# Performance work log

Measured on AMD Instinct MI355X. Metric: run time of the kernel, lower is better.

## Reference

```python
import jax, jax.numpy as jnp
import numpy as np
import math

B, D, S, H = 4, 1024, 2048, 16


def setup_inputs() -> dict:
    key = jax.random.key(0)
    ks = jax.random.split(key, 9)
    scale = 0.02
    return {
        "x": jax.random.normal(ks[0], (B, D, S), dtype=jnp.float32),
        "Wq": jax.random.normal(ks[1], (D, D), dtype=jnp.float32) * scale,
        "bq": jnp.zeros((D,), dtype=jnp.float32),
        "Wk": jax.random.normal(ks[2], (D, D), dtype=jnp.float32) * scale,
        "bk": jnp.zeros((D,), dtype=jnp.float32),
        "Wv": jax.random.normal(ks[3], (D, D), dtype=jnp.float32) * scale,
        "bv": jnp.zeros((D,), dtype=jnp.float32),
        "Wo": jax.random.normal(ks[4], (D, D), dtype=jnp.float32) * scale,
        "bo": jnp.zeros((D,), dtype=jnp.float32),
        "num_heads": H,
    }


def _positional_encoding(d_model, seq_len):
    # pe[0::2, :] = sin(pos * denom), pe[1::2, :] = cos(pos * denom)
    pos = jnp.arange(seq_len, dtype=jnp.float32)[None, :]            # [1, S]
    denom = jnp.exp(jnp.arange(0, d_model, 2, dtype=jnp.float32)
                    * (-math.log(10000.0) / d_model))[:, None]        # [D/2, 1]
    angles = pos * denom                                              # [D/2, S]
    pe = jnp.zeros((d_model, seq_len), dtype=jnp.float32)
    pe = pe.at[0::2, :].set(jnp.sin(angles))
    pe = pe.at[1::2, :].set(jnp.cos(angles))
    return pe


def reference(x, Wq, bq, Wk, bk, Wv, bv, Wo, bo, num_heads):
    b, d_model, s = x.shape
    head_dim = d_model // num_heads
    x = x + _positional_encoding(d_model, s)[None, :, :]  # broadcast over batch
    x = jnp.transpose(x, (0, 2, 1))                       # [B, S, D]
    q = x @ Wq.T + bq
    k = x @ Wk.T + bk
    v = x @ Wv.T + bv
    # [B, S, H, hd] -> [B, H, S, hd]
    q = q.reshape(b, s, num_heads, head_dim).transpose(0, 2, 1, 3)
    k = k.reshape(b, s, num_heads, head_dim).transpose(0, 2, 1, 3)
    v = v.reshape(b, s, num_heads, head_dim).transpose(0, 2, 1, 3)
    scores = jnp.einsum('bhqd,bhkd->bhqk', q, k) / jnp.sqrt(
        jnp.asarray(head_dim, dtype=jnp.float32))
    attn = jax.nn.softmax(scores, axis=-1)
    out = jnp.einsum('bhqk,bhkd->bhqd', attn, v)          # [B, H, S, hd]
    out = out.transpose(0, 2, 1, 3).reshape(b, s, d_model)
    out = out @ Wo.T + bo
    return jnp.transpose(out, (0, 2, 1))                  # [B, D, S]
```

## Files before the change

kernel.cpp:

```cpp
#include <hip/hip_runtime.h>


typedef __bf16 bf16;
typedef __attribute__((ext_vector_type(8))) __bf16 bf16x8;
typedef __attribute__((ext_vector_type(4))) __bf16 bf16x4;
typedef __attribute__((ext_vector_type(4))) float f32x4;

#define NB 4
#define ND 1024
#define NS 2048
#define NH 16
#define NM 8192

__device__ __forceinline__ void gld16(const void* g, void* l) {
  __builtin_amdgcn_global_load_lds((__attribute__((address_space(1))) void*)g,
                                   (__attribute__((address_space(3))) void*)l, 16, 0, 0);
}

__device__ __forceinline__ int swz4(int r) { return (r + (r >> 2)) & 3; }

__device__ __forceinline__ float exp2_fast(float x) {
#if __has_builtin(__builtin_amdgcn_exp2f)
  return __builtin_amdgcn_exp2f(x);
#else
  return exp2f(x);
#endif
}

__global__ __launch_bounds__(256) void prep_x_kernel(const float* __restrict__ x,
                                                     bf16* __restrict__ xT) {
  __shared__ float t[32][33];
  const int tx = threadIdx.x, ty = threadIdx.y;
  const int s0 = blockIdx.x * 32, d0 = blockIdx.y * 32, b = blockIdx.z;
#pragma unroll
  for (int i = 0; i < 4; ++i) {
    const int rr = ty + i * 8;
    const int d = d0 + rr, s = s0 + tx;
    const float freq = __expf(-(float)(d >> 1) * 0.01798894603980689f);
    const float ang = (float)s * freq;
    const float pe = (d & 1) ? cosf(ang) : sinf(ang);
    t[rr][tx] = x[((size_t)b * ND + d) * NS + s] + pe;
  }
  __syncthreads();
#pragma unroll
  for (int i = 0; i < 4; ++i) {
    const int a = ty + i * 8;
    xT[((size_t)b * NS + s0 + a) * ND + d0 + tx] = (bf16)t[tx][a];
  }
}

__global__ __launch_bounds__(256) void prep_w_kernel(const float* __restrict__ Wq,
                                                     const float* __restrict__ Wk,
                                                     const float* __restrict__ Wv,
                                                     const float* __restrict__ Wo,
                                                     bf16* __restrict__ Wqkv,
                                                     bf16* __restrict__ WoB) {
  const size_t t = (size_t)blockIdx.x * blockDim.x + threadIdx.x;
  const size_t i = t * 4;
  const float* src;
  bf16* dst;
  size_t off;
  if (i < (size_t)3 * 1024 * 1024) {
    const int sel = (int)(i >> 20);
    src = sel == 0 ? Wq : (sel == 1 ? Wk : Wv);
    off = i - ((size_t)sel << 20);
    dst = Wqkv + i;
  } else {
    src = Wo;
    off = i - ((size_t)3 << 20);
    dst = WoB + off;
  }
  const f32x4 v = *(const f32x4*)(src + off);
  bf16x4 o;
  o[0] = (bf16)v[0];
  o[1] = (bf16)v[1];
  o[2] = (bf16)v[2];
  o[3] = (bf16)v[3];
  *(bf16x4*)dst = o;
}

__device__ __forceinline__ void gemm_tile_128(const bf16* __restrict__ A,
                                              const bf16* __restrict__ Bm,
                                              int tm, int tn, bf16* ldsA, bf16* ldsB,
                                              f32x4 acc[4][4]) {
  const int tid = threadIdx.x;
  const int lane = tid & 63, wave = tid >> 6;
  const int wm = wave >> 1, wn = wave & 1;
  const int rl = lane & 15, quad = lane >> 4;
  const int sw = swz4(rl);
  int r0[2], c0[2], ld0[2];
#pragma unroll
  for (int j = 0; j < 2; ++j) {
    const int chunk = wave * 2 + j;
    const int o = chunk * 1024 + lane * 16;
    const int r = o >> 6;
    r0[j] = r;
    c0[j] = (((o >> 4) & 3) ^ swz4(r)) * 8;
    ld0[j] = chunk * 1024;
  }
  for (int kt = 0; kt < 1024; kt += 32) {
#pragma unroll
    for (int j = 0; j < 2; ++j) {
      gld16(A + (size_t)(tm + r0[j]) * 1024 + kt + c0[j], (char*)ldsA + ld0[j]);
      gld16(Bm + (size_t)(tn + r0[j]) * 1024 + kt + c0[j], (char*)ldsB + ld0[j]);
    }
    __syncthreads();
    bf16x8 af[4], bfr[4];
#pragma unroll
    for (int i = 0; i < 4; ++i) {
      const int ra = wm * 64 + i * 16 + rl;
      af[i] = *(const bf16x8*)((const char*)ldsA + ra * 64 + ((quad ^ sw) * 16));
      const int rb = wn * 64 + i * 16 + rl;
      bfr[i] = *(const bf16x8*)((const char*)ldsB + rb * 64 + ((quad ^ sw) * 16));
    }
#pragma unroll
    for (int i = 0; i < 4; ++i)
#pragma unroll
      for (int j = 0; j < 4; ++j)
        acc[i][j] = __builtin_amdgcn_mfma_f32_16x16x32_bf16(af[i], bfr[j], acc[i][j], 0, 0, 0);
    __syncthreads();
  }
}

__global__ __launch_bounds__(256, 2) void gemm_qkv_kernel(
    const bf16* __restrict__ xT, const bf16* __restrict__ Wqkv,
    const float* __restrict__ bq, const float* __restrict__ bk,
    const float* __restrict__ bv, bf16* __restrict__ Q, bf16* __restrict__ Kb,
    bf16* __restrict__ VT) {
  __shared__ bf16 ldsA[128 * 32], ldsB[128 * 32];
  const int tm = blockIdx.x * 128, tn = blockIdx.y * 128;
  f32x4 acc[4][4];
  const f32x4 z = {0.f, 0.f, 0.f, 0.f};
#pragma unroll
  for (int i = 0; i < 4; ++i)
#pragma unroll
    for (int j = 0; j < 4; ++j) acc[i][j] = z;
  gemm_tile_128(xT, Wqkv, tm, tn, ldsA, ldsB, acc);
  const int lane = threadIdx.x & 63, wave = threadIdx.x >> 6;
  const int wm = wave >> 1, wn = wave & 1;
  const int rl = lane & 15, quad = lane >> 4;
  const float QSCALE = 0.18033688011112042f;
#pragma unroll
  for (int j = 0; j < 4; ++j) {
    const int n = tn + wn * 64 + j * 16 + rl;
    const int which = n >> 10;
    const int nl = n & 1023;
    const int h = nl >> 6, d = nl & 63;
    const float bias = (which == 0 ? bq : which == 1 ? bk : bv)[nl];
#pragma unroll
    for (int i = 0; i < 4; ++i) {
      const int m0 = tm + wm * 64 + i * 16 + quad * 4;
      const int b = m0 >> 11, s0 = m0 & 2047;
      const size_t bh = (size_t)(b * 16 + h);
      if (which == 2) {
        bf16x4 pk;
#pragma unroll
        for (int r = 0; r < 4; ++r) pk[r] = (bf16)(acc[i][j][r] + bias);
        *(bf16x4*)(VT + ((size_t)bh * 64 + d) * 2048 + s0) = pk;
      } else {
#pragma unroll
        for (int r = 0; r < 4; ++r) {
          const float v = acc[i][j][r] + bias;
          const int s = s0 + r;
          if (which == 0)
            Q[(bh * 2048 + s) * 64 + d] = (bf16)(v * QSCALE);
          else
            Kb[(bh * 2048 + s) * 64 + d] = (bf16)v;
        }
      }
    }
  }
}

__global__ __launch_bounds__(256, 2) void attn_kernel(const bf16* __restrict__ Q,
                                                      const bf16* __restrict__ Kb,
                                                      const bf16* __restrict__ VT,
                                                      bf16* __restrict__ AO) {
  __shared__ __align__(16) char smem[65536];
  char* ldsK = smem;
  char* ldsV = smem + 16384;
  char* ldsP = smem + 32768;
  const int tid = threadIdx.x;
  const int lane = tid & 63, wave = tid >> 6;
  const int rl = lane & 15, quad = lane >> 4;
  const int bh = blockIdx.y;
  const int q0 = blockIdx.x * 256;
  const bf16* Qb = Q + ((size_t)bh * 2048 + q0) * 64;
  const bf16* Kbb = Kb + (size_t)bh * 2048 * 64;
  const bf16* Vb = VT + (size_t)bh * 64 * 2048;
  const int o0 = wave * 1024 + lane * 16, o1 = o0 + 4096;
  const int ra = o0 >> 7, rb = o1 >> 7;
  const int ca = (((o0 >> 4) & 7) ^ (ra & 7)) * 16;
  const int cb = (((o1 >> 4) & 7) ^ (rb & 7)) * 16;
  gld16((const char*)Kbb + (size_t)ra * 128 + ca, ldsK + wave * 1024);
  gld16((const char*)Kbb + (size_t)rb * 128 + cb, ldsK + wave * 1024 + 4096);
  gld16((const char*)Vb + (size_t)ra * 4096 + ca, ldsV + wave * 1024);
  gld16((const char*)Vb + (size_t)rb * 4096 + cb, ldsV + wave * 1024 + 4096);
  bf16x8 qf[4][2];
#pragma unroll
  for (int i = 0; i < 4; ++i)
#pragma unroll
    for (int ks = 0; ks < 2; ++ks)
      qf[i][ks] = *(const bf16x8*)(Qb + (wave * 64 + i * 16 + rl) * 64 + ks * 32 + quad * 8);
  f32x4 o_acc[4][4], lacc[4];
  const f32x4 z = {0.f, 0.f, 0.f, 0.f};
#pragma unroll
  for (int i = 0; i < 4; ++i) {
    lacc[i] = z;
#pragma unroll
    for (int j = 0; j < 4; ++j) o_acc[i][j] = z;
  }
  const bf16 oneb = (bf16)1.0f;
  const bf16x8 onesb = {oneb, oneb, oneb, oneb, oneb, oneb, oneb, oneb};
  char* Pw = ldsP + wave * 8192;
  int buf = 0;
  for (int kt = 0; kt < 2048; kt += 64, buf ^= 1) {
    __syncthreads();
    if (kt + 64 < 2048) {
      const int nb = (buf ^ 1) * 8192;
      gld16((const char*)Kbb + (size_t)(kt + 64 + ra) * 128 + ca, ldsK + nb + wave * 1024);
      gld16((const char*)Kbb + (size_t)(kt + 64 + rb) * 128 + cb,
            ldsK + nb + wave * 1024 + 4096);
      gld16((const char*)Vb + (size_t)ra * 4096 + (size_t)(kt + 64) * 2 + ca,
            ldsV + nb + wave * 1024);
      gld16((const char*)Vb + (size_t)rb * 4096 + (size_t)(kt + 64) * 2 + cb,
            ldsV + nb + wave * 1024 + 4096);
    }
    f32x4 sacc[4][4];
#pragma unroll
    for (int jk = 0; jk < 4; ++jk)
#pragma unroll
      for (int i = 0; i < 4; ++i) sacc[jk][i] = z;
#pragma unroll
    for (int ks = 0; ks < 2; ++ks) {
#pragma unroll
      for (int jk = 0; jk < 4; ++jk) {
        const bf16x8 kf = *(const bf16x8*)(ldsK + buf * 8192 + (jk * 16 + rl) * 128 +
                                           (((ks * 4 + quad) ^ (rl & 7)) * 16));
#pragma unroll
        for (int i = 0; i < 4; ++i)
          sacc[jk][i] =
              __builtin_amdgcn_mfma_f32_16x16x32_bf16(kf, qf[i][ks], sacc[jk][i], 0, 0, 0);
      }
    }
#pragma unroll
    for (int i = 0; i < 4; ++i)
#pragma unroll
      for (int jk = 0; jk < 4; ++jk) {
        bf16x4 pk;
#pragma unroll
        for (int r = 0; r < 4; ++r) pk[r] = (bf16)exp2_fast(sacc[jk][i][r]);
        *(bf16x4*)(Pw + (i * 16 + rl) * 128 +
                   (((jk * 2 + (quad >> 1)) ^ (rl & 7)) * 16) + (quad & 1) * 8) = pk;
      }
    asm volatile("s_waitcnt lgkmcnt(0)" ::: "memory");
#pragma unroll
    for (int ks = 0; ks < 2; ++ks) {
      bf16x8 pf[4];
#pragma unroll
      for (int i = 0; i < 4; ++i)
        pf[i] = *(const bf16x8*)(Pw + (i * 16 + rl) * 128 +
                                 (((ks * 4 + quad) ^ (rl & 7)) * 16));
#pragma unroll
      for (int i = 0; i < 4; ++i)
        lacc[i] = __builtin_amdgcn_mfma_f32_16x16x32_bf16(pf[i], onesb, lacc[i], 0, 0, 0);
#pragma unroll
      for (int j = 0; j < 4; ++j) {
        const bf16x8 vf = *(const bf16x8*)(ldsV + buf * 8192 + (j * 16 + rl) * 128 +
                                           (((ks * 4 + quad) ^ (rl & 7)) * 16));
#pragma unroll
        for (int i = 0; i < 4; ++i)
          o_acc[i][j] =
              __builtin_amdgcn_mfma_f32_16x16x32_bf16(pf[i], vf, o_acc[i][j], 0, 0, 0);
      }
    }
  }
  const int b = bh >> 4, h = bh & 15;
#pragma unroll
  for (int i = 0; i < 4; ++i) {
    f32x4 linv;
#pragma unroll
    for (int r = 0; r < 4; ++r) linv[r] = __builtin_amdgcn_rcpf(lacc[i][r]);
#pragma unroll
    for (int j = 0; j < 4; ++j)
#pragma unroll
      for (int r = 0; r < 4; ++r) {
        const int s = q0 + wave * 64 + i * 16 + quad * 4 + r;
        const int d = h * 64 + j * 16 + rl;
        AO[((size_t)b * 2048 + s) * 1024 + d] = (bf16)(o_acc[i][j][r] * linv[r]);
      }
  }
}

__global__ __launch_bounds__(256, 2) void gemm_out_kernel(const bf16* __restrict__ AO,
                                                          const bf16* __restrict__ WoB,
                                                          const float* __restrict__ bo,
                                                          float* __restrict__ out) {
  __shared__ bf16 ldsA[128 * 32], ldsB[128 * 32];
  const int tm = blockIdx.x * 128, tn = blockIdx.y * 128;
  f32x4 acc[4][4];
  const f32x4 z = {0.f, 0.f, 0.f, 0.f};
#pragma unroll
  for (int i = 0; i < 4; ++i)
#pragma unroll
    for (int j = 0; j < 4; ++j) acc[i][j] = z;
  gemm_tile_128(AO, WoB, tm, tn, ldsA, ldsB, acc);
  const int lane = threadIdx.x & 63, wave = threadIdx.x >> 6;
  const int wm = wave >> 1, wn = wave & 1;
  const int rl = lane & 15, quad = lane >> 4;
#pragma unroll
  for (int j = 0; j < 4; ++j) {
    const int n = tn + wn * 64 + j * 16 + rl;
    const float bias = bo[n];
#pragma unroll
    for (int i = 0; i < 4; ++i) {
      const int m0 = tm + wm * 64 + i * 16 + quad * 4;
      const int b = m0 >> 11, s = m0 & 2047;
      f32x4 v = acc[i][j];
      v[0] += bias;
      v[1] += bias;
      v[2] += bias;
      v[3] += bias;
      *(f32x4*)(out + ((size_t)(b * 1024 + n)) * 2048 + s) = v;
    }
  }
}

extern "C" void kernel_launch(void* const* d_in, const int* in_sizes, int n_in,
                              void* d_out, int out_size, void* d_ws, size_t ws_size,
                              hipStream_t stream) {
  const float* x = (const float*)d_in[0];
  const float* Wq = (const float*)d_in[1];
  const float* bq = (const float*)d_in[2];
  const float* Wk = (const float*)d_in[3];
  const float* bk = (const float*)d_in[4];
  const float* Wv = (const float*)d_in[5];
  const float* bv = (const float*)d_in[6];
  const float* Wo = (const float*)d_in[7];
  const float* bo = (const float*)d_in[8];
  float* out = (float*)d_out;

  char* p = (char*)d_ws;
  bf16* xT = (bf16*)p;
  p += (size_t)NM * ND * 2;
  bf16* Wqkv = (bf16*)p;
  p += (size_t)3 * ND * ND * 2;
  bf16* WoB = (bf16*)p;
  p += (size_t)ND * ND * 2;
  bf16* Qb = (bf16*)p;
  p += (size_t)NM * ND * 2;
  bf16* Kbf = (bf16*)p;
  p += (size_t)NM * ND * 2;
  bf16* VTb = (bf16*)p;
  p += (size_t)NM * ND * 2;
  bf16* AO = xT;

  prep_x_kernel<<<dim3(NS / 32, ND / 32, NB), dim3(32, 8), 0, stream>>>(x, xT);
  prep_w_kernel<<<dim3(4096), dim3(256), 0, stream>>>(Wq, Wk, Wv, Wo, Wqkv, WoB);
  gemm_qkv_kernel<<<dim3(NM / 128, 3072 / 128), dim3(256), 0, stream>>>(
      xT, Wqkv, bq, bk, bv, Qb, Kbf, VTb);
  attn_kernel<<<dim3(NS / 256, NB * NH), dim3(256), 0, stream>>>(Qb, Kbf, VTb, AO);
  gemm_out_kernel<<<dim3(NM / 128, ND / 128), dim3(256), 0, stream>>>(AO, WoB, bo, out);
}
```

Measured before the change: 286.1 us.

## Keep softmax probabilities in registers and use transposed PV MFMA in attention

The attention kernel no longer round-trips the exp'd scores through LDS. It computes S^T tiles so the MFMA output layout feeds directly as the B operand of a 16x16x16 bf16 MFMA computing O^T = V^T P^T, and it accumulates row sums with VALU adds plus cross-lane shuffles instead of a ones-vector MFMA. LDS use drops from 64KB to 32KB, which may raise occupancy, and the grid axes are swapped so blocks of the same query tile sit near each other. The output stores are vectorised as 4-element bf16 writes. The trade-off is the smaller-K MFMA (16 instead of 32), more PV instructions, and higher register pressure from holding P.

```diff
diff --git a/kernel.cpp b/kernel.cpp
--- a/kernel.cpp
+++ b/kernel.cpp
@@ -5,6 +5,7 @@
 typedef __attribute__((ext_vector_type(8))) __bf16 bf16x8;
 typedef __attribute__((ext_vector_type(4))) __bf16 bf16x4;
 typedef __attribute__((ext_vector_type(4))) float f32x4;
+typedef __attribute__((ext_vector_type(4))) short s16x4;
 
 #define NB 4
 #define ND 1024
@@ -176,15 +177,14 @@
                                                       const bf16* __restrict__ Kb,
                                                       const bf16* __restrict__ VT,
                                                       bf16* __restrict__ AO) {
-  __shared__ __align__(16) char smem[65536];
+  __shared__ __align__(16) char smem[32768];
   char* ldsK = smem;
   char* ldsV = smem + 16384;
-  char* ldsP = smem + 32768;
   const int tid = threadIdx.x;
   const int lane = tid & 63, wave = tid >> 6;
   const int rl = lane & 15, quad = lane >> 4;
-  const int bh = blockIdx.y;
-  const int q0 = blockIdx.x * 256;
+  const int bh = blockIdx.x;
+  const int q0 = blockIdx.y * 256;
   const bf16* Qb = Q + ((size_t)bh * 2048 + q0) * 64;
   const bf16* Kbb = Kb + (size_t)bh * 2048 * 64;
   const bf16* Vb = VT + (size_t)bh * 64 * 2048;
@@ -202,17 +202,15 @@
 #pragma unroll
     for (int ks = 0; ks < 2; ++ks)
       qf[i][ks] = *(const bf16x8*)(Qb + (wave * 64 + i * 16 + rl) * 64 + ks * 32 + quad * 8);
-  f32x4 o_acc[4][4], lacc[4];
+  f32x4 o_acc[4][4];
+  f32x4 l4[4];
   const f32x4 z = {0.f, 0.f, 0.f, 0.f};
 #pragma unroll
   for (int i = 0; i < 4; ++i) {
-    lacc[i] = z;
+    l4[i] = z;
 #pragma unroll
     for (int j = 0; j < 4; ++j) o_acc[i][j] = z;
   }
-  const bf16 oneb = (bf16)1.0f;
-  const bf16x8 onesb = {oneb, oneb, oneb, oneb, oneb, oneb, oneb, oneb};
-  char* Pw = ldsP + wave * 8192;
   int buf = 0;
   for (int kt = 0; kt < 2048; kt += 64, buf ^= 1) {
     __syncthreads();
@@ -226,69 +224,62 @@
       gld16((const char*)Vb + (size_t)rb * 4096 + (size_t)(kt + 64) * 2 + cb,
             ldsV + nb + wave * 1024 + 4096);
     }
-    f32x4 sacc[4][4];
-#pragma unroll
-    for (int jk = 0; jk < 4; ++jk)
-#pragma unroll
-      for (int i = 0; i < 4; ++i) sacc[jk][i] = z;
-#pragma unroll
-    for (int ks = 0; ks < 2; ++ks) {
-#pragma unroll
-      for (int jk = 0; jk < 4; ++jk) {
+    s16x4 pb[4][4];
+#pragma unroll
+    for (int jk = 0; jk < 4; ++jk) {
+      f32x4 sacc[4];
+#pragma unroll
+      for (int i = 0; i < 4; ++i) sacc[i] = z;
+#pragma unroll
+      for (int ks = 0; ks < 2; ++ks) {
         const bf16x8 kf = *(const bf16x8*)(ldsK + buf * 8192 + (jk * 16 + rl) * 128 +
                                            (((ks * 4 + quad) ^ (rl & 7)) * 16));
 #pragma unroll
         for (int i = 0; i < 4; ++i)
-          sacc[jk][i] =
-              __builtin_amdgcn_mfma_f32_16x16x32_bf16(kf, qf[i][ks], sacc[jk][i], 0, 0, 0);
+          sacc[i] =
+              __builtin_amdgcn_mfma_f32_16x16x32_bf16(kf, qf[i][ks], sacc[i], 0, 0, 0);
       }
-    }
-#pragma unroll
-    for (int i = 0; i < 4; ++i)
-#pragma unroll
-      for (int jk = 0; jk < 4; ++jk) {
+#pragma unroll
+      for (int i = 0; i < 4; ++i) {
+        f32x4 e;
+#pragma unroll
+        for (int r = 0; r < 4; ++r) e[r] = exp2_fast(sacc[i][r]);
+        l4[i] += e;
         bf16x4 pk;
 #pragma unroll
-        for (int r = 0; r < 4; ++r) pk[r] = (bf16)exp2_fast(sacc[jk][i][r]);
-        *(bf16x4*)(Pw + (i * 16 + rl) * 128 +
-                   (((jk * 2 + (quad >> 1)) ^ (rl & 7)) * 16) + (quad & 1) * 8) = pk;
+        for (int r = 0; r < 4; ++r) pk[r] = (bf16)e[r];
+        pb[jk][i] = __builtin_bit_cast(s16x4, pk);
       }
-    asm volatile("s_waitcnt lgkmcnt(0)" ::: "memory");
-#pragma unroll
-    for (int ks = 0; ks < 2; ++ks) {
-      bf16x8 pf[4];
-#pragma unroll
-      for (int i = 0; i < 4; ++i)
-        pf[i] = *(const bf16x8*)(Pw + (i * 16 + rl) * 128 +
-                                 (((ks * 4 + quad) ^ (rl & 7)) * 16));
-#pragma unroll
-      for (int i = 0; i < 4; ++i)
-        lacc[i] = __builtin_amdgcn_mfma_f32_16x16x32_bf16(pf[i], onesb, lacc[i], 0, 0, 0);
-#pragma unroll
-      for (int j = 0; j < 4; ++j) {
-        const bf16x8 vf = *(const bf16x8*)(ldsV + buf * 8192 + (j * 16 + rl) * 128 +
-                                           (((ks * 4 + quad) ^ (rl & 7)) * 16));
-#pragma unroll
-        for (int i = 0; i < 4; ++i)
-          o_acc[i][j] =
-              __builtin_amdgcn_mfma_f32_16x16x32_bf16(pf[i], vf, o_acc[i][j], 0, 0, 0);
+    }
+#pragma unroll
+    for (int ki = 0; ki < 4; ++ki) {
+#pragma unroll
+      for (int dt = 0; dt < 4; ++dt) {
+        const s16x4 vf = *(const s16x4*)(ldsV + buf * 8192 + (dt * 16 + rl) * 128 +
+                                         (((ki * 2 + (quad >> 1)) ^ (rl & 7)) * 16) +
+                                         (quad & 1) * 8);
+#pragma unroll
+        for (int qt = 0; qt < 4; ++qt)
+          o_acc[dt][qt] = __builtin_amdgcn_mfma_f32_16x16x16bf16_1k(vf, pb[ki][qt],
+                                                                    o_acc[dt][qt], 0, 0, 0);
       }
     }
   }
   const int b = bh >> 4, h = bh & 15;
 #pragma unroll
-  for (int i = 0; i < 4; ++i) {
-    f32x4 linv;
-#pragma unroll
-    for (int r = 0; r < 4; ++r) linv[r] = __builtin_amdgcn_rcpf(lacc[i][r]);
-#pragma unroll
-    for (int j = 0; j < 4; ++j)
-#pragma unroll
-      for (int r = 0; r < 4; ++r) {
-        const int s = q0 + wave * 64 + i * 16 + quad * 4 + r;
-        const int d = h * 64 + j * 16 + rl;
-        AO[((size_t)b * 2048 + s) * 1024 + d] = (bf16)(o_acc[i][j][r] * linv[r]);
-      }
+  for (int qt = 0; qt < 4; ++qt) {
+    float s = l4[qt][0] + l4[qt][1] + l4[qt][2] + l4[qt][3];
+    s += __shfl_xor(s, 16);
+    s += __shfl_xor(s, 32);
+    const float linv = __builtin_amdgcn_rcpf(s);
+    const size_t row = ((size_t)b * 2048 + q0 + wave * 64 + qt * 16 + rl) * 1024;
+#pragma unroll
+    for (int dt = 0; dt < 4; ++dt) {
+      bf16x4 ov;
+#pragma unroll
+      for (int r = 0; r < 4; ++r) ov[r] = (bf16)(o_acc[dt][qt][r] * linv);
+      *(bf16x4*)(AO + row + h * 64 + dt * 16 + quad * 4) = ov;
+    }
   }
 }
 
@@ -359,6 +350,6 @@
   prep_w_kernel<<<dim3(4096), dim3(256), 0, stream>>>(Wq, Wk, Wv, Wo, Wqkv, WoB);
   gemm_qkv_kernel<<<dim3(NM / 128, 3072 / 128), dim3(256), 0, stream>>>(
       xT, Wqkv, bq, bk, bv, Qb, Kbf, VTb);
-  attn_kernel<<<dim3(NS / 256, NB * NH), dim3(256), 0, stream>>>(Qb, Kbf, VTb, AO);
+  attn_kernel<<<dim3(NB * NH, NS / 256), dim3(256), 0, stream>>>(Qb, Kbf, VTb, AO);
   gemm_out_kernel<<<dim3(NM / 128, ND / 128), dim3(256), 0, stream>>>(AO, WoB, bo, out);
 }
```

New measurement: 289.4 us. About the same (+1.2%).

## Deepen GEMM K-tile to 64, interleave QK exp, and swap attention grid order

Applied to the files above, without the earlier changes.

The shared GEMM tile now loads a K-slab of 64 instead of 32 per iteration, using an 8-way XOR swizzle on 128-byte rows. This halves the number of barrier pairs per tile at the cost of twice the LDS per block. In the attention kernel, each 16x16 score tile is computed and exponentiated immediately instead of holding all 16 score accumulators first, which lowers register pressure. The attention grid is also transposed so that consecutive blocks take different heads for the same query range, which changes how K/V reads are spread across the cache.

```diff
diff --git a/kernel.cpp b/kernel.cpp
--- a/kernel.cpp
+++ b/kernel.cpp
@@ -16,8 +16,6 @@
   __builtin_amdgcn_global_load_lds((__attribute__((address_space(1))) void*)g,
                                    (__attribute__((address_space(3))) void*)l, 16, 0, 0);
 }
-
-__device__ __forceinline__ int swz4(int r) { return (r + (r >> 2)) & 3; }
 
 __device__ __forceinline__ float exp2_fast(float x) {
 #if __has_builtin(__builtin_amdgcn_exp2f)
@@ -87,37 +85,40 @@
   const int lane = tid & 63, wave = tid >> 6;
   const int wm = wave >> 1, wn = wave & 1;
   const int rl = lane & 15, quad = lane >> 4;
-  const int sw = swz4(rl);
-  int r0[2], c0[2], ld0[2];
-#pragma unroll
-  for (int j = 0; j < 2; ++j) {
-    const int chunk = wave * 2 + j;
-    const int o = chunk * 1024 + lane * 16;
-    const int r = o >> 6;
+  int r0[4], c0[4];
+#pragma unroll
+  for (int j = 0; j < 4; ++j) {
+    const int o = (wave * 4 + j) * 1024 + lane * 16;
+    const int r = o >> 7;
     r0[j] = r;
-    c0[j] = (((o >> 4) & 3) ^ swz4(r)) * 8;
-    ld0[j] = chunk * 1024;
-  }
-  for (int kt = 0; kt < 1024; kt += 32) {
-#pragma unroll
-    for (int j = 0; j < 2; ++j) {
-      gld16(A + (size_t)(tm + r0[j]) * 1024 + kt + c0[j], (char*)ldsA + ld0[j]);
-      gld16(Bm + (size_t)(tn + r0[j]) * 1024 + kt + c0[j], (char*)ldsB + ld0[j]);
+    c0[j] = ((((o >> 4) & 7) ^ (r & 7)) * 8);
+  }
+  for (int kt = 0; kt < 1024; kt += 64) {
+#pragma unroll
+    for (int j = 0; j < 4; ++j) {
+      gld16(A + (size_t)(tm + r0[j]) * 1024 + kt + c0[j], (char*)ldsA + (wave * 4 + j) * 1024);
+      gld16(Bm + (size_t)(tn + r0[j]) * 1024 + kt + c0[j], (char*)ldsB + (wave * 4 + j) * 1024);
     }
     __syncthreads();
-    bf16x8 af[4], bfr[4];
-#pragma unroll
-    for (int i = 0; i < 4; ++i) {
-      const int ra = wm * 64 + i * 16 + rl;
-      af[i] = *(const bf16x8*)((const char*)ldsA + ra * 64 + ((quad ^ sw) * 16));
-      const int rb = wn * 64 + i * 16 + rl;
-      bfr[i] = *(const bf16x8*)((const char*)ldsB + rb * 64 + ((quad ^ sw) * 16));
-    }
-#pragma unroll
-    for (int i = 0; i < 4; ++i)
-#pragma unroll
-      for (int j = 0; j < 4; ++j)
-        acc[i][j] = __builtin_amdgcn_mfma_f32_16x16x32_bf16(af[i], bfr[j], acc[i][j], 0, 0, 0);
+#pragma unroll
+    for (int kk = 0; kk < 2; ++kk) {
+      bf16x8 af[4], bfr[4];
+#pragma unroll
+      for (int i = 0; i < 4; ++i) {
+        const int ra = wm * 64 + i * 16 + rl;
+        af[i] = *(const bf16x8*)((const char*)ldsA + ra * 128 +
+                                 (((kk * 4 + quad) ^ (rl & 7)) * 16));
+        const int rb = wn * 64 + i * 16 + rl;
+        bfr[i] = *(const bf16x8*)((const char*)ldsB + rb * 128 +
+                                  (((kk * 4 + quad) ^ (rl & 7)) * 16));
+      }
+#pragma unroll
+      for (int i = 0; i < 4; ++i)
+#pragma unroll
+        for (int j = 0; j < 4; ++j)
+          acc[i][j] =
+              __builtin_amdgcn_mfma_f32_16x16x32_bf16(af[i], bfr[j], acc[i][j], 0, 0, 0);
+    }
     __syncthreads();
   }
 }
@@ -127,7 +128,7 @@
     const float* __restrict__ bq, const float* __restrict__ bk,
     const float* __restrict__ bv, bf16* __restrict__ Q, bf16* __restrict__ Kb,
     bf16* __restrict__ VT) {
-  __shared__ bf16 ldsA[128 * 32], ldsB[128 * 32];
+  __shared__ bf16 ldsA[128 * 64], ldsB[128 * 64];
   const int tm = blockIdx.x * 128, tn = blockIdx.y * 128;
   f32x4 acc[4][4];
   const f32x4 z = {0.f, 0.f, 0.f, 0.f};
@@ -183,8 +184,8 @@
   const int tid = threadIdx.x;
   const int lane = tid & 63, wave = tid >> 6;
   const int rl = lane & 15, quad = lane >> 4;
-  const int bh = blockIdx.y;
-  const int q0 = blockIdx.x * 256;
+  const int bh = blockIdx.x;
+  const int q0 = blockIdx.y * 256;
   const bf16* Qb = Q + ((size_t)bh * 2048 + q0) * 64;
   const bf16* Kbb = Kb + (size_t)bh * 2048 * 64;
   const bf16* Vb = VT + (size_t)bh * 64 * 2048;
@@ -201,7 +202,8 @@
   for (int i = 0; i < 4; ++i)
 #pragma unroll
     for (int ks = 0; ks < 2; ++ks)
-      qf[i][ks] = *(const bf16x8*)(Qb + (wave * 64 + i * 16 + rl) * 64 + ks * 32 + quad * 8);
+      qf[i][ks] =
+          *(const bf16x8*)(Qb + (wave * 64 + i * 16 + rl) * 64 + ks * 32 + quad * 8);
   f32x4 o_acc[4][4], lacc[4];
   const f32x4 z = {0.f, 0.f, 0.f, 0.f};
 #pragma unroll
@@ -226,33 +228,26 @@
       gld16((const char*)Vb + (size_t)rb * 4096 + (size_t)(kt + 64) * 2 + cb,
             ldsV + nb + wave * 1024 + 4096);
     }
-    f32x4 sacc[4][4];
-#pragma unroll
-    for (int jk = 0; jk < 4; ++jk)
-#pragma unroll
-      for (int i = 0; i < 4; ++i) sacc[jk][i] = z;
-#pragma unroll
-    for (int ks = 0; ks < 2; ++ks) {
-#pragma unroll
-      for (int jk = 0; jk < 4; ++jk) {
-        const bf16x8 kf = *(const bf16x8*)(ldsK + buf * 8192 + (jk * 16 + rl) * 128 +
-                                           (((ks * 4 + quad) ^ (rl & 7)) * 16));
-#pragma unroll
-        for (int i = 0; i < 4; ++i)
-          sacc[jk][i] =
-              __builtin_amdgcn_mfma_f32_16x16x32_bf16(kf, qf[i][ks], sacc[jk][i], 0, 0, 0);
-      }
-    }
-#pragma unroll
-    for (int i = 0; i < 4; ++i)
-#pragma unroll
-      for (int jk = 0; jk < 4; ++jk) {
+    const char* Kbase = ldsK + buf * 8192;
+    const char* Vbase = ldsV + buf * 8192;
+#pragma unroll
+    for (int jk = 0; jk < 4; ++jk) {
+      const bf16x8 kf0 =
+          *(const bf16x8*)(Kbase + (jk * 16 + rl) * 128 + ((quad ^ (rl & 7)) * 16));
+      const bf16x8 kf1 =
+          *(const bf16x8*)(Kbase + (jk * 16 + rl) * 128 + (((4 + quad) ^ (rl & 7)) * 16));
+#pragma unroll
+      for (int i = 0; i < 4; ++i) {
+        f32x4 s = z;
+        s = __builtin_amdgcn_mfma_f32_16x16x32_bf16(kf0, qf[i][0], s, 0, 0, 0);
+        s = __builtin_amdgcn_mfma_f32_16x16x32_bf16(kf1, qf[i][1], s, 0, 0, 0);
         bf16x4 pk;
 #pragma unroll
-        for (int r = 0; r < 4; ++r) pk[r] = (bf16)exp2_fast(sacc[jk][i][r]);
-        *(bf16x4*)(Pw + (i * 16 + rl) * 128 +
-                   (((jk * 2 + (quad >> 1)) ^ (rl & 7)) * 16) + (quad & 1) * 8) = pk;
-      }
+        for (int r = 0; r < 4; ++r) pk[r] = (bf16)exp2_fast(s[r]);
+        *(bf16x4*)(Pw + (i * 16 + rl) * 128 + (((jk * 2 + (quad >> 1)) ^ (rl & 7)) * 16) +
+                   (quad & 1) * 8) = pk;
+      }
+    }
     asm volatile("s_waitcnt lgkmcnt(0)" ::: "memory");
 #pragma unroll
     for (int ks = 0; ks < 2; ++ks) {
@@ -266,7 +261,7 @@
         lacc[i] = __builtin_amdgcn_mfma_f32_16x16x32_bf16(pf[i], onesb, lacc[i], 0, 0, 0);
 #pragma unroll
       for (int j = 0; j < 4; ++j) {
-        const bf16x8 vf = *(const bf16x8*)(ldsV + buf * 8192 + (j * 16 + rl) * 128 +
+        const bf16x8 vf = *(const bf16x8*)(Vbase + (j * 16 + rl) * 128 +
                                            (((ks * 4 + quad) ^ (rl & 7)) * 16));
 #pragma unroll
         for (int i = 0; i < 4; ++i)
@@ -296,7 +291,7 @@
                                                           const bf16* __restrict__ WoB,
                                                           const float* __restrict__ bo,
                                                           float* __restrict__ out) {
-  __shared__ bf16 ldsA[128 * 32], ldsB[128 * 32];
+  __shared__ bf16 ldsA[128 * 64], ldsB[128 * 64];
   const int tm = blockIdx.x * 128, tn = blockIdx.y * 128;
   f32x4 acc[4][4];
   const f32x4 z = {0.f, 0.f, 0.f, 0.f};
@@ -359,6 +354,6 @@
   prep_w_kernel<<<dim3(4096), dim3(256), 0, stream>>>(Wq, Wk, Wv, Wo, Wqkv, WoB);
   gemm_qkv_kernel<<<dim3(NM / 128, 3072 / 128), dim3(256), 0, stream>>>(
       xT, Wqkv, bq, bk, bv, Qb, Kbf, VTb);
-  attn_kernel<<<dim3(NS / 256, NB * NH), dim3(256), 0, stream>>>(Qb, Kbf, VTb, AO);
+  attn_kernel<<<dim3(NB * NH, NS / 256), dim3(256), 0, stream>>>(Qb, Kbf, VTb, AO);
   gemm_out_kernel<<<dim3(NM / 128, ND / 128), dim3(256), 0, stream>>>(AO, WoB, bo, out);
 }
```

Measured after the change: 271.2 us. -5.2%, faster.
